# Kernel tuning notes

Hardware: AMD Instinct MI355X
Metric: run time of the kernel (lower is better)

Reference implementation:

```python
import jax, jax.numpy as jnp
import numpy as np

B, S, D, H = 4, 2048, 1024, 16
HD = D // H
EPS = 1e-5
MASKED_BIAS = -10000.0

def setup_inputs() -> dict:
    key = jax.random.key(0)
    ks = jax.random.split(key, 12)
    sd = 0.02
    return {
        "hidden_states": jax.random.normal(ks[0], (B, S, D), jnp.float32),
        "Wq": jax.random.normal(ks[1], (D, D), jnp.float32) * sd,
        "bq": jnp.zeros((D,), jnp.float32),
        "Wk": jax.random.normal(ks[2], (D, D), jnp.float32) * sd,
        "bk": jnp.zeros((D,), jnp.float32),
        "Wv": jax.random.normal(ks[3], (D, D), jnp.float32) * sd,
        "bv": jnp.zeros((D,), jnp.float32),
        "Wp": jax.random.normal(ks[4], (D, D), jnp.float32) * sd,
        "bp": jnp.zeros((D,), jnp.float32),
        "ln_g": jnp.ones((D,), jnp.float32),
        "ln_b": jnp.zeros((D,), jnp.float32),
    }

def reference(hidden_states, Wq, bq, Wk, bk, Wv, bv, Wp, bp, ln_g, ln_b):
    x = hidden_states  # [B,S,D]
    # QKV projections (nn.Linear: x @ W^T + b; here W stored as [D,D], use x@W)
    q = x @ Wq + bq
    k = x @ Wk + bk
    v = x @ Wv + bv
    # split heads -> [B,H,S,HD]
    def split(t):
        return t.reshape(B, S, H, HD).transpose(0, 2, 1, 3)
    q, k, v = split(q), split(k), split(v)
    # scaled scores [B,H,S,S]
    scores = jnp.einsum("bhqd,bhkd->bhqk", q, k) / jnp.float32(np.sqrt(HD))
    causal = jnp.tril(jnp.ones((S, S), bool))
    scores = jnp.where(causal[None, None], scores, jnp.float32(MASKED_BIAS))
    attn = jax.nn.softmax(scores, axis=-1)
    out = jnp.einsum("bhqk,bhkd->bhqd", attn, v)
    # merge heads -> [B,S,D]
    out = out.transpose(0, 2, 1, 3).reshape(B, S, D)
    out = out @ Wp + bp
    # residual + layernorm
    y = out + x
    mu = jnp.mean(y, axis=-1, keepdims=True)
    var = jnp.var(y, axis=-1, keepdims=True)
    y = (y - mu) * jax.lax.rsqrt(var + EPS) * ln_g + ln_b
    return y
```

## Files before the change

kernel.cpp:

```cpp
#include <hip/hip_runtime.h>
#include <math.h>

#define B_  4
#define S_  2048
#define D_  1024
#define H_  16
#define HD_ 64
#define M_  (B_*S_)

typedef unsigned int  uint;
typedef unsigned short ushort;

typedef __attribute__((ext_vector_type(8))) short bf16x8;
typedef __attribute__((ext_vector_type(4))) float f32x4;

#if __has_builtin(__builtin_amdgcn_exp2f)
#define EXP2(x) __builtin_amdgcn_exp2f(x)
#else
#define EXP2(x) exp2f(x)
#endif

#define GPTR(p) (const __attribute__((address_space(1))) void*)(p)
#define LPTR(p) (__attribute__((address_space(3))) void*)(p)

__device__ __forceinline__ ushort f2bf(float x) {
    uint u = __float_as_uint(x);
    u += 0x7FFFu + ((u >> 16) & 1u);
    return (ushort)(u >> 16);
}
__device__ __forceinline__ uint pack2bf(float a, float b) {
    uint ua = __float_as_uint(a); ua += 0x7FFFu + ((ua >> 16) & 1u);
    uint ub = __float_as_uint(b); ub += 0x7FFFu + ((ub >> 16) & 1u);
    return (ua >> 16) | (ub & 0xFFFF0000u);
}
__device__ __forceinline__ uint cvtpk2bf(float a, float b) {
    uint r;
    asm("v_cvt_pk_bf16_f32 %0, %1, %2" : "=v"(r) : "v"(a), "v"(b));
    return r;
}

__global__ __launch_bounds__(256) void prep(const float* __restrict__ x,
                                            ushort* __restrict__ xb,
                                            const float* __restrict__ Wq,
                                            const float* __restrict__ Wk,
                                            const float* __restrict__ Wv,
                                            const float* __restrict__ Wp,
                                            ushort* __restrict__ wtq,
                                            ushort* __restrict__ wtk,
                                            ushort* __restrict__ wtv,
                                            ushort* __restrict__ wtp) {
    __shared__ float t[32][33];
    const int tid = threadIdx.x;
    if (blockIdx.z == 0) {
        const int idx = blockIdx.x * 256 + tid;
        const float4* p = (const float4*)(x + (size_t)idx * 8);
        float4 a = p[0], b = p[1];
        uint4 o;
        o.x = pack2bf(a.x, a.y); o.y = pack2bf(a.z, a.w);
        o.z = pack2bf(b.x, b.y); o.w = pack2bf(b.z, b.w);
        ((uint4*)xb)[idx] = o;
    } else {
        const int w = blockIdx.x >> 10;
        const int sub = blockIdx.x & 1023;
        const float* W = (w == 0) ? Wq : (w == 1) ? Wk : (w == 2) ? Wv : Wp;
        ushort* Wt     = (w == 0) ? wtq : (w == 1) ? wtk : (w == 2) ? wtv : wtp;
        const int nb = (sub & 31) * 32, kb = (sub >> 5) * 32;
        #pragma unroll
        for (int l = 0; l < 4; ++l) {
            int idx = tid + l * 256;
            int r = idx >> 5, c = idx & 31;
            t[r][c] = W[(size_t)(kb + r) * D_ + nb + c];
        }
        __syncthreads();
        #pragma unroll
        for (int l = 0; l < 4; ++l) {
            int idx = tid + l * 256;
            int nr = idx >> 5, kc = idx & 31;
            Wt[(size_t)(nb + nr) * D_ + kb + kc] = f2bf(t[kc][nr]);
        }
    }
}

struct QLds {
    ushort As[3][128 * 32];
    ushort Bs[3][256 * 32];
};

#define QSTAGE(tile_, buf_) do {                                                \
    const int ko_ = (tile_) * 64;                                               \
    __builtin_amdgcn_global_load_lds(GPTR(Ab + ko_ + sgA),                      \
        LPTR(&L.As[buf_][wave * 512]), 16, 0, 0);                               \
    __builtin_amdgcn_global_load_lds(GPTR(Bb + ko_ + sgB0),                     \
        LPTR(&L.Bs[buf_][wave * 512]), 16, 0, 0);                               \
    __builtin_amdgcn_global_load_lds(GPTR(Bb + ko_ + sgB1),                     \
        LPTR(&L.Bs[buf_][4096 + wave * 512]), 16, 0, 0);                        \
} while (0)

#define QCOMPUTE(buf_) do {                                                     \
    const char* As_ = (const char*)L.As[buf_];                                  \
    const char* Bs_ = (const char*)L.Bs[buf_];                                  \
    bf16x8 af[4], bf[4];                                                        \
    _Pragma("unroll")                                                           \
    for (int i_ = 0; i_ < 4; ++i_)                                              \
        af[i_] = *(const bf16x8*)(As_ + (wm + 16 * i_ + fr) * 64 + ((fq * 16) ^ xrw)); \
    _Pragma("unroll")                                                           \
    for (int j_ = 0; j_ < 4; ++j_)                                              \
        bf[j_] = *(const bf16x8*)(Bs_ + (wn + 16 * j_ + fr) * 64 + ((fq * 16) ^ xrw)); \
    __builtin_amdgcn_s_setprio(1);                                              \
    _Pragma("unroll")                                                           \
    for (int i_ = 0; i_ < 4; ++i_)                                              \
        _Pragma("unroll")                                                       \
        for (int j_ = 0; j_ < 4; ++j_)                                          \
            acc[i_][j_] = SWAP                                                  \
                ? __builtin_amdgcn_mfma_f32_16x16x32_bf16(bf[j_], af[i_], acc[i_][j_], 0, 0, 0) \
                : __builtin_amdgcn_mfma_f32_16x16x32_bf16(af[i_], bf[j_], acc[i_][j_], 0, 0, 0); \
    __builtin_amdgcn_s_setprio(0);                                              \
} while (0)

#define QSTEP(buf_, sbuf_, stile_) do {                                         \
    asm volatile("s_waitcnt vmcnt(3)" ::: "memory");                            \
    __builtin_amdgcn_s_barrier();                                               \
    QSTAGE(stile_, sbuf_);                                                      \
    QCOMPUTE(buf_);                                                             \
} while (0)

template <bool SWAP>
__device__ __forceinline__ void qcore(QLds& L,
                                      const ushort* __restrict__ A,
                                      const ushort* __restrict__ Bt,
                                      f32x4 acc[4][4], int m0, int n0) {
    const int tid  = threadIdx.x;
    const int wave = tid >> 6, lane = tid & 63;
    const int wm = (wave >> 2) * 64;
    const int wn = (wave & 3) * 64;
    const int fr = lane & 15, fq = lane >> 4;
    const int xrw = ((fr >> 1) & 3) << 4;

    int sgA, sgB0, sgB1;
    {
        int o = tid * 16;
        int r = o >> 6, c = o & 63;
        sgA = r * (D_ * 2) + (c ^ (((r >> 1) & 3) << 4));
        sgB0 = sgA;
        o = 8192 + tid * 16;
        r = o >> 6; c = o & 63;
        sgB1 = r * (D_ * 2) + (c ^ (((r >> 1) & 3) << 4));
    }

    #pragma unroll
    for (int i = 0; i < 4; ++i)
        #pragma unroll
        for (int j = 0; j < 4; ++j) acc[i][j] = (f32x4){0.f, 0.f, 0.f, 0.f};

    const char* Ab = (const char*)A + (size_t)m0 * (D_ * 2);
    const char* Bb = (const char*)Bt + (size_t)n0 * (D_ * 2);

    QSTAGE(0, 0);
    QSTAGE(1, 1);

    #pragma unroll 1
    for (int it = 0; it < 10; ++it) {
        const int t0 = it * 3;
        QSTEP(0, 2, t0 + 2);
        QSTEP(1, 0, t0 + 3);
        QSTEP(2, 1, t0 + 4);
    }
    asm volatile("s_waitcnt vmcnt(3)" ::: "memory");
    __builtin_amdgcn_s_barrier();
    QCOMPUTE(0);
    asm volatile("s_waitcnt vmcnt(0)" ::: "memory");
    __builtin_amdgcn_s_barrier();
    QCOMPUTE(1);
}

__global__ __launch_bounds__(512, 4) void gemm_qkvt(const ushort* __restrict__ xb,
                                                    const ushort* __restrict__ wtq,
                                                    const ushort* __restrict__ wtk,
                                                    const ushort* __restrict__ wtv,
                                                    const float* __restrict__ bq,
                                                    const float* __restrict__ bk,
                                                    const float* __restrict__ bv,
                                                    ushort* __restrict__ qb,
                                                    ushort* __restrict__ kb,
                                                    ushort* __restrict__ vtb) {
    __shared__ __align__(16) QLds L;
    const int z = blockIdx.z;
    const int lane = threadIdx.x & 63, wave = threadIdx.x >> 6;
    const int wm = (wave >> 2) * 64, wn = (wave & 3) * 64;
    const int cc = lane & 15, fq = lane >> 4;
    const int m0 = blockIdx.x * 128, n0 = blockIdx.y * 256;
    f32x4 acc[4][4];

    if (z < 2) {
        qcore<true>(L, xb, z ? wtk : wtq, acc, m0, n0);
        const float* bias = z ? bk : bq;
        ushort* C = z ? kb : qb;
        const float sc = z ? 1.0f : 0.18033688f;
        #pragma unroll
        for (int j = 0; j < 4; ++j) {
            const int f0 = n0 + wn + 16 * j + fq * 4;
            const float4 bs4 = *(const float4*)&bias[f0];
            const int h = f0 >> 6, hd = f0 & 63;
            #pragma unroll
            for (int i = 0; i < 4; ++i) {
                const int token = m0 + wm + 16 * i + cc;
                const int bb = token >> 11, s = token & 2047;
                const float v0 = (acc[i][j][0] + bs4.x) * sc;
                const float v1 = (acc[i][j][1] + bs4.y) * sc;
                const float v2 = (acc[i][j][2] + bs4.z) * sc;
                const float v3 = (acc[i][j][3] + bs4.w) * sc;
                uint2 w; w.x = pack2bf(v0, v1); w.y = pack2bf(v2, v3);
                *(uint2*)&C[(((size_t)bb * H_ + h) * S_ + s) * HD_ + hd] = w;
            }
        }
    } else {
        qcore<false>(L, xb, wtv, acc, m0, n0);
        #pragma unroll
        for (int i = 0; i < 4; ++i) {
            const int t0 = m0 + wm + 16 * i + fq * 4;
            const int bb = t0 >> 11, s = t0 & 2047;
            #pragma unroll
            for (int j = 0; j < 4; ++j) {
                const int f = n0 + wn + 16 * j + cc;
                const float bs = bv[f];
                const int h = f >> 6, hd = f & 63;
                uint2 w;
                w.x = pack2bf(acc[i][j][0] + bs, acc[i][j][1] + bs);
                w.y = pack2bf(acc[i][j][2] + bs, acc[i][j][3] + bs);
                *(uint2*)&vtb[(((size_t)bb * H_ + h) * HD_ + hd) * S_ + s] = w;
            }
        }
    }
}

#define GM 128
#define GN 128
#define GK 32

struct PLds {
    ushort As[2][GM * GK];
    ushort Bs[2][GN * GK];
};

#define PSTAGE(koff_, buf_) do {                                                \
    _Pragma("unroll")                                                           \
    for (int it_ = 0; it_ < 2; ++it_) {                                         \
        __builtin_amdgcn_global_load_lds(GPTR(Ab + (koff_) + sg[it_]),          \
            LPTR(&L.As[buf_][(it_ * 256 + wave * 64) * 8]), 16, 0, 0);          \
        __builtin_amdgcn_global_load_lds(GPTR(Bb + (koff_) + sg[it_]),          \
            LPTR(&L.Bs[buf_][(it_ * 256 + wave * 64) * 8]), 16, 0, 0);          \
    } } while (0)

__device__ __forceinline__ void pgemm_core(PLds& L,
                                           const ushort* __restrict__ A,
                                           const ushort* __restrict__ Bt,
                                           f32x4 acc[4][4], int m0, int n0) {
    const int tid  = threadIdx.x;
    const int wave = tid >> 6, lane = tid & 63;
    const int wm = (wave >> 1) * 64, wn = (wave & 1) * 64;
    const int fr = lane & 15, fq = lane >> 4;
    const int xrw = ((fr >> 1) & 3) << 4;

    int sg[2];
    #pragma unroll
    for (int it = 0; it < 2; ++it) {
        const int o = (it * 256 + tid) * 16;
        const int r = o >> 6, c = o & 63;
        sg[it] = r * (D_ * 2) + (c ^ (((r >> 1) & 3) << 4));
    }

    #pragma unroll
    for (int i = 0; i < 4; ++i)
        #pragma unroll
        for (int j = 0; j < 4; ++j) acc[i][j] = (f32x4){0.f, 0.f, 0.f, 0.f};

    const char* Ab = (const char*)A + (size_t)m0 * (D_ * 2);
    const char* Bb = (const char*)Bt + (size_t)n0 * (D_ * 2);

    PSTAGE(0, 0);
    __syncthreads();

    int cur = 0;
    for (int k0 = 0; k0 < D_; k0 += GK) {
        if (k0 + GK < D_) PSTAGE((k0 + GK) * 2, cur ^ 1);

        bf16x8 af[4], bfr[4];
        #pragma unroll
        for (int i = 0; i < 4; ++i)
            af[i] = *(const bf16x8*)((const char*)L.As[cur] + (wm + 16 * i + fr) * 64 + ((fq * 16) ^ xrw));
        #pragma unroll
        for (int j = 0; j < 4; ++j)
            bfr[j] = *(const bf16x8*)((const char*)L.Bs[cur] + (wn + 16 * j + fr) * 64 + ((fq * 16) ^ xrw));
        #pragma unroll
        for (int i = 0; i < 4; ++i)
            #pragma unroll
            for (int j = 0; j < 4; ++j)
                acc[i][j] = __builtin_amdgcn_mfma_f32_16x16x32_bf16(af[i], bfr[j], acc[i][j], 0, 0, 0);

        __syncthreads();
        cur ^= 1;
    }
}

__global__ __launch_bounds__(256) void gemm_p(const ushort* __restrict__ A,
                                              const ushort* __restrict__ Bt,
                                              const float* __restrict__ bias,
                                              const float* __restrict__ xres,
                                              float* __restrict__ C) {
    __shared__ __align__(16) PLds L;
    const int m0 = blockIdx.y * GM, n0 = blockIdx.x * GN;
    f32x4 acc[4][4];
    pgemm_core(L, A, Bt, acc, m0, n0);

    const int lane = threadIdx.x & 63, wave = threadIdx.x >> 6;
    const int wm = (wave >> 1) * 64, wn = (wave & 1) * 64;
    const int cr = (lane >> 4) * 4, cc = lane & 15;
    #pragma unroll
    for (int j = 0; j < 4; ++j) {
        const int col = n0 + wn + 16 * j + cc;
        const float bs = bias[col];
        #pragma unroll
        for (int i = 0; i < 4; ++i)
            #pragma unroll
            for (int r = 0; r < 4; ++r) {
                const size_t idx = (size_t)(m0 + wm + 16 * i + cr + r) * D_ + col;
                C[idx] = acc[i][j][r] + bs + xres[idx];
            }
    }
}

#define PST 72

#define STAGE(kt_, buf_) do {                                                   \
    const int kn_ = (kt_) * 64;                                                 \
    __builtin_amdgcn_global_load_lds(                                           \
        GPTR((const char*)kbase + (size_t)kn_ * 128 + kg),                      \
        LPTR(&Ks[buf_][wave * 512]), 16, 0, 0);                                 \
    __builtin_amdgcn_global_load_lds(                                           \
        GPTR((const char*)vbase + (size_t)kn_ * 2 + vg),                        \
        LPTR(&Vs[buf_][wave * 512]), 16, 0, 0);                                 \
} while (0)

__global__ __launch_bounds__(512, 4) void attn_mfma(const ushort* __restrict__ qb,
                                                    const ushort* __restrict__ kb,
                                                    const ushort* __restrict__ vtb,
                                                    ushort* __restrict__ ob) {
    __shared__ __align__(16) ushort Ks[2][64 * 64];
    __shared__ __align__(16) ushort Vs[2][64 * 64];
    __shared__ __align__(16) ushort Pp[8][16 * PST];

    const int tid = threadIdx.x, wave = tid >> 6, lane = tid & 63;
    const int fr = lane & 15, fq = lane >> 4;
    const int hb = blockIdx.x;
    const int p  = blockIdx.y;
    const int b = hb >> 4, h = hb & 15;
    const size_t bh = (size_t)b * H_ + h;
    const ushort* qbase = qb + bh * S_ * HD_;
    const ushort* kbase = kb + bh * S_ * HD_;
    const ushort* vbase = vtb + bh * HD_ * S_;
    ushort* PpW = Pp[wave];
    const int xrw = (fr & 7) << 4;

    int kg, vg;
    {
        const int o = tid * 16;
        const int r = o >> 7, cS = o & 127;
        kg = r * 128 + (cS ^ ((r & 7) << 4));
        vg = r * (S_ * 2) + (cS ^ ((r & 7) << 4));
    }

    for (int phase = 0; phase < 2; ++phase) {
        const int chunk = phase ? p : (15 - p);
        const int q0 = chunk * 128;
        const int wq0 = q0 + wave * 16;
        const int qrow = wq0 + fr;
        const int ntile = 2 * (chunk + 1);

        bf16x8 qf[2];
        #pragma unroll
        for (int kk = 0; kk < 2; ++kk)
            qf[kk] = *(const bf16x8*)&qbase[(size_t)qrow * HD_ + kk * 32 + fq * 8];

        f32x4 ot[4];
        #pragma unroll
        for (int mt = 0; mt < 4; ++mt) ot[mt] = (f32x4){0.f, 0.f, 0.f, 0.f};
        float lp = 0.f;

        int cur = 0;
        STAGE(0, 0);
        __syncthreads();

        for (int t = 0; t < ntile; ++t) {
            if (t + 1 < ntile) STAGE(t + 1, cur ^ 1);
            const ushort* Kb = Ks[cur];
            const ushort* Vb = Vs[cur];
            const int k0 = t * 64;

            f32x4 st[4];
            #pragma unroll
            for (int mt = 0; mt < 4; ++mt) st[mt] = (f32x4){0.f, 0.f, 0.f, 0.f};

            if (t < ntile - 2) {
                #pragma unroll
                for (int kk = 0; kk < 2; ++kk) {
                    bf16x8 kf[4];
                    #pragma unroll
                    for (int mt = 0; mt < 4; ++mt)
                        kf[mt] = *(const bf16x8*)((const char*)Kb + (mt * 16 + fr) * 128 + ((kk * 64 + fq * 16) ^ xrw));
                    __builtin_amdgcn_s_setprio(1);
                    #pragma unroll
                    for (int mt = 0; mt < 4; ++mt)
                        st[mt] = __builtin_amdgcn_mfma_f32_16x16x32_bf16(kf[mt], qf[kk], st[mt], 0, 0, 0);
                    __builtin_amdgcn_s_setprio(0);
                }
                #pragma unroll
                for (int mt = 0; mt < 4; ++mt) {
                    float pr[4];
                    #pragma unroll
                    for (int r = 0; r < 4; ++r) pr[r] = EXP2(st[mt][r]);
                    lp += (pr[0] + pr[1]) + (pr[2] + pr[3]);
                    uint2 w;
                    w.x = cvtpk2bf(pr[0], pr[1]);
                    w.y = cvtpk2bf(pr[2], pr[3]);
                    *(uint2*)&PpW[fr * PST + mt * 16 + fq * 4] = w;
                }
                #pragma unroll
                for (int kk = 0; kk < 2; ++kk) {
                    bf16x8 vf[4];
                    #pragma unroll
                    for (int mt = 0; mt < 4; ++mt)
                        vf[mt] = *(const bf16x8*)((const char*)Vb + (mt * 16 + fr) * 128 + ((kk * 64 + fq * 16) ^ xrw));
                    bf16x8 pf = *(const bf16x8*)&PpW[fr * PST + kk * 32 + fq * 8];
                    __builtin_amdgcn_s_setprio(1);
                    #pragma unroll
                    for (int mt = 0; mt < 4; ++mt)
                        ot[mt] = __builtin_amdgcn_mfma_f32_16x16x32_bf16(vf[mt], pf, ot[mt], 0, 0, 0);
                    __builtin_amdgcn_s_setprio(0);
                }
            } else {
                #pragma unroll
                for (int kk = 0; kk < 2; ++kk) {
                    bf16x8 kf[4];
                    #pragma unroll
                    for (int mt = 0; mt < 4; ++mt)
                        kf[mt] = *(const bf16x8*)((const char*)Kb + (mt * 16 + fr) * 128 + ((kk * 64 + fq * 16) ^ xrw));
                    #pragma unroll
                    for (int mt = 0; mt < 4; ++mt)
                        if (k0 + mt * 16 <= wq0 + 15)
                            st[mt] = __builtin_amdgcn_mfma_f32_16x16x32_bf16(kf[mt], qf[kk], st[mt], 0, 0, 0);
                }
                #pragma unroll
                for (int mt = 0; mt < 4; ++mt) {
                    const int kb0 = k0 + mt * 16 + fq * 4;
                    float pr[4];
                    #pragma unroll
                    for (int r = 0; r < 4; ++r) {
                        const float e = EXP2(st[mt][r]);
                        pr[r] = (kb0 + r > qrow) ? 0.f : e;
                    }
                    lp += (pr[0] + pr[1]) + (pr[2] + pr[3]);
                    uint2 w;
                    w.x = cvtpk2bf(pr[0], pr[1]);
                    w.y = cvtpk2bf(pr[2], pr[3]);
                    *(uint2*)&PpW[fr * PST + mt * 16 + fq * 4] = w;
                }
                #pragma unroll
                for (int kk = 0; kk < 2; ++kk) {
                    if (k0 + kk * 32 <= wq0 + 15) {
                        bf16x8 vf[4];
                        #pragma unroll
                        for (int mt = 0; mt < 4; ++mt)
                            vf[mt] = *(const bf16x8*)((const char*)Vb + (mt * 16 + fr) * 128 + ((kk * 64 + fq * 16) ^ xrw));
                        bf16x8 pf = *(const bf16x8*)&PpW[fr * PST + kk * 32 + fq * 8];
                        #pragma unroll
                        for (int mt = 0; mt < 4; ++mt)
                            ot[mt] = __builtin_amdgcn_mfma_f32_16x16x32_bf16(vf[mt], pf, ot[mt], 0, 0, 0);
                    }
                }
            }
            __syncthreads();
            cur ^= 1;
        }

        float l = lp;
        l += __shfl_xor(l, 16);
        l += __shfl_xor(l, 32);
        const float inv = 1.0f / l;
        #pragma unroll
        for (int mt = 0; mt < 4; ++mt) {
            uint2 w;
            w.x = cvtpk2bf(ot[mt][0] * inv, ot[mt][1] * inv);
            w.y = cvtpk2bf(ot[mt][2] * inv, ot[mt][3] * inv);
            *(uint2*)&ob[((size_t)b * S_ + qrow) * D_ + h * HD_ + mt * 16 + fq * 4] = w;
        }
    }
}

__global__ __launch_bounds__(256) void resln(float* __restrict__ out,
                                             const float* __restrict__ g,
                                             const float* __restrict__ bb) {
    __shared__ float red[256];
    const int row = blockIdx.x, tid = threadIdx.x;
    const size_t off = (size_t)row * D_ + tid * 4;

    float4 y = *(const float4*)&out[off];

    float sum = y.x + y.y + y.z + y.w;
    red[tid] = sum;
    __syncthreads();
    #pragma unroll
    for (int st = 128; st > 0; st >>= 1) {
        if (tid < st) red[tid] += red[tid + st];
        __syncthreads();
    }
    const float mu = red[0] * (1.0f / D_);
    __syncthreads();

    float dx = y.x - mu, dy = y.y - mu, dz = y.z - mu, dw = y.w - mu;
    red[tid] = dx * dx + dy * dy + dz * dz + dw * dw;
    __syncthreads();
    #pragma unroll
    for (int st = 128; st > 0; st >>= 1) {
        if (tid < st) red[tid] += red[tid + st];
        __syncthreads();
    }
    const float var = red[0] * (1.0f / D_);
    const float inv = rsqrtf(var + 1e-5f);

    float4 gg = *(const float4*)&g[tid * 4];
    float4 bv = *(const float4*)&bb[tid * 4];
    float4 r;
    r.x = dx * inv * gg.x + bv.x;
    r.y = dy * inv * gg.y + bv.y;
    r.z = dz * inv * gg.z + bv.z;
    r.w = dw * inv * gg.w + bv.w;
    *(float4*)&out[off] = r;
}

extern "C" void kernel_launch(void* const* d_in, const int* in_sizes, int n_in,
                              void* d_out, int out_size, void* d_ws, size_t ws_size,
                              hipStream_t stream) {
    const float* x    = (const float*)d_in[0];
    const float* Wq   = (const float*)d_in[1];
    const float* bq   = (const float*)d_in[2];
    const float* Wk   = (const float*)d_in[3];
    const float* bk   = (const float*)d_in[4];
    const float* Wv   = (const float*)d_in[5];
    const float* bv   = (const float*)d_in[6];
    const float* Wp   = (const float*)d_in[7];
    const float* bp   = (const float*)d_in[8];
    const float* ln_g = (const float*)d_in[9];
    const float* ln_b = (const float*)d_in[10];

    float* out = (float*)d_out;

    char* ws = (char*)d_ws;
    ushort* qb  = (ushort*)ws;
    ushort* kb  = (ushort*)(ws + (size_t)16 * (1 << 20));
    ushort* vtb = (ushort*)(ws + (size_t)32 * (1 << 20));
    ushort* xb  = (ushort*)(ws + (size_t)48 * (1 << 20));
    ushort* ob  = (ushort*)(ws + (size_t)64 * (1 << 20));
    ushort* wtq = (ushort*)(ws + (size_t)80 * (1 << 20));
    ushort* wtk = (ushort*)(ws + (size_t)82 * (1 << 20));
    ushort* wtv = (ushort*)(ws + (size_t)84 * (1 << 20));
    ushort* wtp = (ushort*)(ws + (size_t)86 * (1 << 20));

    prep<<<dim3(4096, 1, 2), 256, 0, stream>>>(x, xb, Wq, Wk, Wv, Wp, wtq, wtk, wtv, wtp);

    gemm_qkvt<<<dim3(M_ / 128, D_ / 256, 3), 512, 0, stream>>>(
        xb, wtq, wtk, wtv, bq, bk, bv, qb, kb, vtb);

    attn_mfma<<<dim3(64, 8), 512, 0, stream>>>(qb, kb, vtb, ob);

    gemm_p<<<dim3(D_ / GN, M_ / GM), 256, 0, stream>>>(ob, wtp, bp, x, out);
    resln<<<M_, 256, 0, stream>>>(out, ln_g, ln_b);
}
```

Baseline: 267.7 us.

## Use 4-wave blocks with 128x64 per-wave tiles in QKV GEMM

The QKV projection GEMM moves from 8 waves per block (each computing 64x64) to 4 waves per block, each computing 128x64 (8x4 MFMA tiles). Each wave now stages more of the tile per step (6 async loads instead of 3), and the waitcnt thresholds are adjusted to match. The aim is to get more MFMA work out of each LDS fragment load and to cut barrier overhead per FLOP. In exchange, accumulator register pressure roughly doubles and there are fewer waves per block to hide latency.

```diff
diff --git a/kernel.cpp b/kernel.cpp
--- a/kernel.cpp
+++ b/kernel.cpp
@@ -88,27 +88,29 @@
 
 #define QSTAGE(tile_, buf_) do {                                                \
     const int ko_ = (tile_) * 64;                                               \
-    __builtin_amdgcn_global_load_lds(GPTR(Ab + ko_ + sgA),                      \
-        LPTR(&L.As[buf_][wave * 512]), 16, 0, 0);                               \
-    __builtin_amdgcn_global_load_lds(GPTR(Bb + ko_ + sgB0),                     \
-        LPTR(&L.Bs[buf_][wave * 512]), 16, 0, 0);                               \
-    __builtin_amdgcn_global_load_lds(GPTR(Bb + ko_ + sgB1),                     \
-        LPTR(&L.Bs[buf_][4096 + wave * 512]), 16, 0, 0);                        \
+    _Pragma("unroll")                                                           \
+    for (int it_ = 0; it_ < 2; ++it_)                                           \
+        __builtin_amdgcn_global_load_lds(GPTR(Ab + ko_ + sgA[it_]),             \
+            LPTR(&L.As[buf_][it_ * 2048 + wave * 512]), 16, 0, 0);              \
+    _Pragma("unroll")                                                           \
+    for (int it_ = 0; it_ < 4; ++it_)                                           \
+        __builtin_amdgcn_global_load_lds(GPTR(Bb + ko_ + sgB[it_]),             \
+            LPTR(&L.Bs[buf_][it_ * 2048 + wave * 512]), 16, 0, 0);              \
 } while (0)
 
 #define QCOMPUTE(buf_) do {                                                     \
     const char* As_ = (const char*)L.As[buf_];                                  \
     const char* Bs_ = (const char*)L.Bs[buf_];                                  \
-    bf16x8 af[4], bf[4];                                                        \
+    bf16x8 af[8], bf[4];                                                        \
     _Pragma("unroll")                                                           \
-    for (int i_ = 0; i_ < 4; ++i_)                                              \
-        af[i_] = *(const bf16x8*)(As_ + (wm + 16 * i_ + fr) * 64 + ((fq * 16) ^ xrw)); \
+    for (int i_ = 0; i_ < 8; ++i_)                                              \
+        af[i_] = *(const bf16x8*)(As_ + (16 * i_ + fr) * 64 + ((fq * 16) ^ xrw)); \
     _Pragma("unroll")                                                           \
     for (int j_ = 0; j_ < 4; ++j_)                                              \
         bf[j_] = *(const bf16x8*)(Bs_ + (wn + 16 * j_ + fr) * 64 + ((fq * 16) ^ xrw)); \
     __builtin_amdgcn_s_setprio(1);                                              \
     _Pragma("unroll")                                                           \
-    for (int i_ = 0; i_ < 4; ++i_)                                              \
+    for (int i_ = 0; i_ < 8; ++i_)                                              \
         _Pragma("unroll")                                                       \
         for (int j_ = 0; j_ < 4; ++j_)                                          \
             acc[i_][j_] = SWAP                                                  \
@@ -118,7 +120,7 @@
 } while (0)
 
 #define QSTEP(buf_, sbuf_, stile_) do {                                         \
-    asm volatile("s_waitcnt vmcnt(3)" ::: "memory");                            \
+    asm volatile("s_waitcnt vmcnt(6)" ::: "memory");                            \
     __builtin_amdgcn_s_barrier();                                               \
     QSTAGE(stile_, sbuf_);                                                      \
     QCOMPUTE(buf_);                                                             \
@@ -128,27 +130,29 @@
 __device__ __forceinline__ void qcore(QLds& L,
                                       const ushort* __restrict__ A,
                                       const ushort* __restrict__ Bt,
-                                      f32x4 acc[4][4], int m0, int n0) {
+                                      f32x4 acc[8][4], int m0, int n0) {
     const int tid  = threadIdx.x;
     const int wave = tid >> 6, lane = tid & 63;
-    const int wm = (wave >> 2) * 64;
-    const int wn = (wave & 3) * 64;
+    const int wn = wave * 64;
     const int fr = lane & 15, fq = lane >> 4;
     const int xrw = ((fr >> 1) & 3) << 4;
 
-    int sgA, sgB0, sgB1;
-    {
-        int o = tid * 16;
-        int r = o >> 6, c = o & 63;
-        sgA = r * (D_ * 2) + (c ^ (((r >> 1) & 3) << 4));
-        sgB0 = sgA;
-        o = 8192 + tid * 16;
-        r = o >> 6; c = o & 63;
-        sgB1 = r * (D_ * 2) + (c ^ (((r >> 1) & 3) << 4));
-    }
-
-    #pragma unroll
-    for (int i = 0; i < 4; ++i)
+    int sgA[2], sgB[4];
+    #pragma unroll
+    for (int it = 0; it < 2; ++it) {
+        const int o = it * 4096 + tid * 16;
+        const int r = o >> 6, c = o & 63;
+        sgA[it] = r * (D_ * 2) + (c ^ (((r >> 1) & 3) << 4));
+    }
+    #pragma unroll
+    for (int it = 0; it < 4; ++it) {
+        const int o = it * 4096 + tid * 16;
+        const int r = o >> 6, c = o & 63;
+        sgB[it] = r * (D_ * 2) + (c ^ (((r >> 1) & 3) << 4));
+    }
+
+    #pragma unroll
+    for (int i = 0; i < 8; ++i)
         #pragma unroll
         for (int j = 0; j < 4; ++j) acc[i][j] = (f32x4){0.f, 0.f, 0.f, 0.f};
 
@@ -165,7 +169,7 @@
         QSTEP(1, 0, t0 + 3);
         QSTEP(2, 1, t0 + 4);
     }
-    asm volatile("s_waitcnt vmcnt(3)" ::: "memory");
+    asm volatile("s_waitcnt vmcnt(6)" ::: "memory");
     __builtin_amdgcn_s_barrier();
     QCOMPUTE(0);
     asm volatile("s_waitcnt vmcnt(0)" ::: "memory");
@@ -173,7 +177,7 @@
     QCOMPUTE(1);
 }
 
-__global__ __launch_bounds__(512, 4) void gemm_qkvt(const ushort* __restrict__ xb,
+__global__ __launch_bounds__(256, 2) void gemm_qkvt(const ushort* __restrict__ xb,
                                                     const ushort* __restrict__ wtq,
                                                     const ushort* __restrict__ wtk,
                                                     const ushort* __restrict__ wtv,
@@ -186,10 +190,10 @@
     __shared__ __align__(16) QLds L;
     const int z = blockIdx.z;
     const int lane = threadIdx.x & 63, wave = threadIdx.x >> 6;
-    const int wm = (wave >> 2) * 64, wn = (wave & 3) * 64;
+    const int wn = wave * 64;
     const int cc = lane & 15, fq = lane >> 4;
     const int m0 = blockIdx.x * 128, n0 = blockIdx.y * 256;
-    f32x4 acc[4][4];
+    f32x4 acc[8][4];
 
     if (z < 2) {
         qcore<true>(L, xb, z ? wtk : wtq, acc, m0, n0);
@@ -202,8 +206,8 @@
             const float4 bs4 = *(const float4*)&bias[f0];
             const int h = f0 >> 6, hd = f0 & 63;
             #pragma unroll
-            for (int i = 0; i < 4; ++i) {
-                const int token = m0 + wm + 16 * i + cc;
+            for (int i = 0; i < 8; ++i) {
+                const int token = m0 + 16 * i + cc;
                 const int bb = token >> 11, s = token & 2047;
                 const float v0 = (acc[i][j][0] + bs4.x) * sc;
                 const float v1 = (acc[i][j][1] + bs4.y) * sc;
@@ -216,8 +220,8 @@
     } else {
         qcore<false>(L, xb, wtv, acc, m0, n0);
         #pragma unroll
-        for (int i = 0; i < 4; ++i) {
-            const int t0 = m0 + wm + 16 * i + fq * 4;
+        for (int i = 0; i < 8; ++i) {
+            const int t0 = m0 + 16 * i + fq * 4;
             const int bb = t0 >> 11, s = t0 & 2047;
             #pragma unroll
             for (int j = 0; j < 4; ++j) {
@@ -567,7 +571,7 @@
 
     prep<<<dim3(4096, 1, 2), 256, 0, stream>>>(x, xb, Wq, Wk, Wv, Wp, wtq, wtk, wtv, wtp);
 
-    gemm_qkvt<<<dim3(M_ / 128, D_ / 256, 3), 512, 0, stream>>>(
+    gemm_qkvt<<<dim3(M_ / 128, D_ / 256, 3), 256, 0, stream>>>(
         xb, wtq, wtk, wtv, bq, bk, bv, qb, kb, vtb);
 
     attn_mfma<<<dim3(64, 8), 512, 0, stream>>>(qb, kb, vtb, ob);
```

Measured after the change: 277.1 us. 3.5% more time.
